# Kernel tuning notes

Measured on AMD Instinct MI355X. Metric: run time of the kernel, lower is better.

The kernel has to match this reference:

```python
import jax, jax.numpy as jnp
import numpy as np

B, H, W, C = 4, 256, 256, 96
NH, WIN = 3, 8
HD = C // NH
HID = 4 * C
SCALE = HD ** -0.5
N = WIN * WIN


def _rel_pos_index(win):
    # matches torch.meshgrid([h, w]) default 'ij' indexing
    coords = np.stack(np.meshgrid(np.arange(win), np.arange(win), indexing='ij'))
    cf = coords.reshape(2, -1)
    rel = (cf[:, :, None] - cf[:, None, :]).transpose(1, 2, 0).astype(np.int64)
    rel[..., 0] += win - 1
    rel[..., 1] += win - 1
    rel[..., 0] *= 2 * win - 1
    return rel.sum(-1)

REL_IDX = jnp.asarray(_rel_pos_index(WIN))


def _ln(x, g, b, eps=1e-5):
    m = x.mean(-1, keepdims=True)
    v = ((x - m) ** 2).mean(-1, keepdims=True)
    return (x - m) * jax.lax.rsqrt(v + eps) * g + b


def setup_inputs() -> dict:
    key = jax.random.key(0)
    ks = jax.random.split(key, 10)
    s = 0.02
    return {
        'x': jax.random.normal(ks[0], (B, H * W, C), jnp.float32),
        'g1': jnp.ones((C,), jnp.float32), 'b1': jnp.zeros((C,), jnp.float32),
        'wq': jax.random.normal(ks[1], (C, C), jnp.float32) * s, 'bq': jnp.zeros((C,), jnp.float32),
        'wkv': jax.random.normal(ks[2], (C, 2 * C), jnp.float32) * s, 'bkv': jnp.zeros((2 * C,), jnp.float32),
        'rpb': jax.random.normal(ks[3], ((2 * WIN - 1) ** 2, NH), jnp.float32) * s,
        'wp': jax.random.normal(ks[4], (C, C), jnp.float32) * s, 'bp': jnp.zeros((C,), jnp.float32),
        'g2': jnp.ones((C,), jnp.float32), 'b2': jnp.zeros((C,), jnp.float32),
        'w1': jax.random.normal(ks[5], (C, HID), jnp.float32) * s, 'bl1': jnp.zeros((HID,), jnp.float32),
        'wdw': jax.random.normal(ks[6], (HID, 1, 3, 3), jnp.float32) * s, 'bdw': jnp.zeros((HID,), jnp.float32),
        'w2': jax.random.normal(ks[7], (HID, C), jnp.float32) * s, 'bl2': jnp.zeros((C,), jnp.float32),
    }


def reference(x, g1, b1, wq, bq, wkv, bkv, rpb, wp, bp, g2, b2, w1, bl1, wdw, bdw, w2, bl2):
    shortcut = x
    xn = _ln(x, g1, b1)
    q = xn @ wq + bq                      # (B, L, C)
    kv = xn @ wkv + bkv                   # (B, L, 2C)

    def windows(t, c):
        t = t.reshape(B, H // WIN, WIN, W // WIN, WIN, c)
        return t.transpose(0, 1, 3, 2, 4, 5).reshape(-1, N, c)

    qw = windows(q, C).reshape(-1, N, NH, HD).transpose(0, 2, 1, 3)     # (nB, NH, N, HD)
    kvw = windows(kv, 2 * C).reshape(-1, N, 2, NH, HD).transpose(2, 0, 3, 1, 4)
    kw, vw = kvw[0], kvw[1]

    attn = jnp.einsum('bhnd,bhmd->bhnm', qw * SCALE, kw)                # (nB, NH, N, N)
    bias = rpb[REL_IDX]                                                  # (N, N, NH)
    attn = attn + bias.transpose(2, 0, 1)[None]
    # shift_size=0 -> shift mask is identically zero; adding it is a no-op
    attn = jax.nn.softmax(attn, axis=-1)
    y = jnp.einsum('bhnm,bhmd->bhnd', attn, vw)
    y = y.transpose(0, 2, 1, 3).reshape(-1, N, C)
    y = y @ wp + bp

    # window_reverse
    y = y.reshape(B, H // WIN, W // WIN, WIN, WIN, C)
    y = y.transpose(0, 1, 3, 2, 4, 5).reshape(B, H * W, C)
    x = shortcut + y

    # LeFF: linear1 + GELU -> depthwise 3x3 conv + GELU -> linear2
    xn2 = _ln(x, g2, b2)
    h = jax.nn.gelu(xn2 @ w1 + bl1, approximate=False)                  # (B, L, HID)
    h = h.reshape(B, H, W, HID).transpose(0, 3, 1, 2)                    # NCHW
    h = jax.lax.conv_general_dilated(
        h, wdw, window_strides=(1, 1), padding=((1, 1), (1, 1)),
        dimension_numbers=('NCHW', 'OIHW', 'NCHW'), feature_group_count=HID)
    h = jax.nn.gelu(h + bdw[None, :, None, None], approximate=False)
    h = h.transpose(0, 2, 3, 1).reshape(B, H * W, HID)
    h = h @ w2 + bl2
    return x + h
```

## Files before the change

kernel.cpp:

```cpp
#include <hip/hip_runtime.h>
#include <math.h>


typedef __attribute__((ext_vector_type(8))) short bf16x8;
typedef __attribute__((ext_vector_type(4))) float f32x4;
typedef __attribute__((ext_vector_type(2))) float f32x2;

#define MFMA(a, b, c) __builtin_amdgcn_mfma_f32_16x16x32_bf16((a), (b), (c), 0, 0, 0)

#define WQ_T 0
#define WKV_T 18
#define WP_T 54
#define W1_T 72
#define W2_T 144
#define NTILES_TOT 216

__device__ __forceinline__ unsigned short f2bf(float f) {
  union { float f; unsigned u; } v; v.f = f;
  unsigned r = v.u + 0x7FFFu + ((v.u >> 16) & 1u);
  return (unsigned short)(r >> 16);
}
__device__ __forceinline__ float asf(unsigned u) {
  union { unsigned u; float f; } v; v.u = u; return v.f;
}
__device__ __forceinline__ unsigned cvtpk_bf16(float lo, float hi) {
  unsigned r;
  asm("v_cvt_pk_bf16_f32 %0, %1, %2" : "=v"(r) : "v"(lo), "v"(hi));
  return r;
}
__device__ __forceinline__ float gelu(float x) {
  float t = x * x;
  float w = x * fmaf(t, -0.07135941f, -1.5957691f);
  float a = __expf(w);
  return x * __builtin_amdgcn_rcpf(1.f + a);
}
__device__ __forceinline__ bf16x8 ldw(const unsigned short* wswz, int tile, int lane) {
  return *(const bf16x8*)(wswz + ((size_t)(tile * 64 + lane)) * 8);
}
__device__ __forceinline__ int xcd_swz(int bid) {
  return (bid & 7) * 512 + (bid >> 3);
}

__global__ void kwconv(const float* __restrict__ wq, const float* __restrict__ wkv,
                       const float* __restrict__ wp, const float* __restrict__ w1,
                       const float* __restrict__ w2, const float* __restrict__ wdw,
                       unsigned short* __restrict__ wswz, float* __restrict__ wdwT) {
  int tid = blockIdx.x * 256 + threadIdx.x;
  if (tid >= NTILES_TOT * 64) {
    int i = tid - NTILES_TOT * 64;
    if (i < 3456) {
      int ch = i % 384, tap = i / 384;
      wdwT[tap * 384 + ch] = wdw[ch * 9 + tap];
    }
    return;
  }
  int e = tid; const float* src; int N, NT;
  if (e < 1152)      { src = wq;  N = 96;  NT = 6; }
  else if (e < 3456) { src = wkv; N = 192; NT = 12; e -= 1152; }
  else if (e < 4608) { src = wp;  N = 96;  NT = 6;  e -= 3456; }
  else if (e < 9216) { src = w1;  N = 384; NT = 24; e -= 4608; }
  else               { src = w2;  N = 96;  NT = 6;  e -= 9216; }
  int lane = e & 63, t = e >> 6;
  int nt = t % NT, kt = t / NT;
  int k0 = kt * 32 + (lane >> 4) * 8;
  int n = nt * 16 + (lane & 15);
  unsigned short* dst = wswz + (size_t)tid * 8;
#pragma unroll
  for (int i = 0; i < 8; ++i) dst[i] = f2bf(src[(size_t)(k0 + i) * N + n]);
}

__global__ __launch_bounds__(256) void kattn(
    const float* __restrict__ x, const float* __restrict__ g1, const float* __restrict__ b1,
    const float* __restrict__ bq, const float* __restrict__ bkv,
    const float* __restrict__ rpb, const float* __restrict__ bp,
    const unsigned short* __restrict__ wswz, float* __restrict__ x2) {
  __shared__ __align__(16) unsigned short sm0[4 * 3 * 64 * 8];
  __shared__ __align__(16) unsigned short sm1[24 * 64 * 8];
  __shared__ __align__(16) unsigned short sm2[3 * 2 * 2 * 64 * 8];

  const int tid = threadIdx.x;
  const int lane = tid & 63, w = tid >> 6;
  const int lrow = lane >> 4, lcol = lane & 15;
  const int wi = xcd_swz(blockIdx.x);
  const int b = wi >> 10, wy = (wi >> 5) & 31, wx = wi & 31;

  long rowoff[4];
#pragma unroll
  for (int r = 0; r < 4; ++r) {
    int m = w * 16 + lrow * 4 + r;
    int gy = wy * 8 + (m >> 3), gx = wx * 8 + (m & 7);
    rowoff[r] = ((long)b * 65536 + gy * 256 + gx) * 96;
  }

  float xv[4][6], xn[4][6], gv[6], bv[6];
#pragma unroll
  for (int nt = 0; nt < 6; ++nt) {
    int c = nt * 16 + lcol;
    gv[nt] = g1[c]; bv[nt] = b1[c];
#pragma unroll
    for (int r = 0; r < 4; ++r) xv[r][nt] = x[rowoff[r] + c];
  }
#pragma unroll
  for (int r = 0; r < 4; ++r) {
    float s = 0.f, sq = 0.f;
#pragma unroll
    for (int nt = 0; nt < 6; ++nt) { float v = xv[r][nt]; s += v; sq += v * v; }
#pragma unroll
    for (int off = 1; off <= 8; off <<= 1) { s += __shfl_xor(s, off, 64); sq += __shfl_xor(sq, off, 64); }
    float mean = s * (1.f / 96.f);
    float var = sq * (1.f / 96.f) - mean * mean;
    float rs = rsqrtf(var + 1e-5f);
#pragma unroll
    for (int nt = 0; nt < 6; ++nt) xn[r][nt] = (xv[r][nt] - mean) * rs * gv[nt] + bv[nt];
  }
#pragma unroll
  for (int r = 0; r < 4; ++r) {
    int mm = lrow * 4 + r;
#pragma unroll
    for (int nt = 0; nt < 6; ++nt) {
      int c = nt * 16 + lcol;
      int kt = c >> 5;
      int lanew = mm + (((c & 31) >> 3) << 4);
      sm0[((w * 3 + kt) * 64 + lanew) * 8 + (c & 7)] = f2bf(xn[r][nt]);
    }
  }
  __syncthreads();

  bf16x8 af[3];
#pragma unroll
  for (int kt = 0; kt < 3; ++kt) af[kt] = *(const bf16x8*)(sm0 + ((w * 3 + kt) * 64 + lane) * 8);
  for (int nt = 0; nt < 18; ++nt) {
    f32x4 acc = {0.f, 0.f, 0.f, 0.f};
#pragma unroll
    for (int kt = 0; kt < 3; ++kt) {
      int tile = (nt < 6) ? (WQ_T + kt * 6 + nt) : (WKV_T + kt * 12 + (nt - 6));
      acc = MFMA(af[kt], ldw(wswz, tile, lane), acc);
    }
    int c = nt * 16 + lcol;
#pragma unroll
    for (int r = 0; r < 4; ++r) {
      int m = w * 16 + lrow * 4 + r;
      float val = acc[r];
      if (c < 96) {
        val = (val + bq[c]) * 0.17677669529663687f;
        int head = c >> 5, d = c & 31;
        sm1[((head * 4 + w) * 64 + (m & 15) + ((d >> 3) << 4)) * 8 + (d & 7)] = f2bf(val);
      } else if (c < 192) {
        int kc = c - 96;
        val += bkv[kc];
        int head = kc >> 5, d = kc & 31;
        sm1[((12 + head * 4 + w) * 64 + (m & 15) + ((d >> 3) << 4)) * 8 + (d & 7)] = f2bf(val);
      } else {
        int vc = c - 192;
        val += bkv[96 + vc];
        int head = vc >> 5, d = vc & 31;
        int ktile = m >> 5, nt2 = d >> 4;
        sm2[(((head * 2 + ktile) * 2 + nt2) * 64 + (d & 15) + (((m & 31) >> 3) << 4)) * 8 + (m & 7)] = f2bf(val);
      }
    }
  }
  __syncthreads();

  f32x4 sc[3][4];
#pragma unroll
  for (int uu = 0; uu < 3; ++uu) {
    int u = w * 3 + uu, head = u >> 2, mtq = u & 3;
    bf16x8 aq = *(const bf16x8*)(sm1 + ((head * 4 + mtq) * 64 + lane) * 8);
#pragma unroll
    for (int nt = 0; nt < 4; ++nt) {
      bf16x8 bk = *(const bf16x8*)(sm1 + ((12 + head * 4 + nt) * 64 + lane) * 8);
      f32x4 z = {0.f, 0.f, 0.f, 0.f};
      sc[uu][nt] = MFMA(aq, bk, z);
    }
  }
  __syncthreads();

#pragma unroll
  for (int uu = 0; uu < 3; ++uu) {
    int u = w * 3 + uu, head = u >> 2, mtq = u & 3;
#pragma unroll
    for (int nt = 0; nt < 4; ++nt) {
      int ktok = nt * 16 + lcol;
#pragma unroll
      for (int r = 0; r < 4; ++r) {
        int qtok = mtq * 16 + lrow * 4 + r;
        int dy = (qtok >> 3) - (ktok >> 3) + 7;
        int dx = (qtok & 7) - (ktok & 7) + 7;
        sc[uu][nt][r] += rpb[(dy * 15 + dx) * 3 + head];
      }
    }
#pragma unroll
    for (int r = 0; r < 4; ++r) {
      float mx = fmaxf(fmaxf(sc[uu][0][r], sc[uu][1][r]), fmaxf(sc[uu][2][r], sc[uu][3][r]));
#pragma unroll
      for (int off = 1; off <= 8; off <<= 1) mx = fmaxf(mx, __shfl_xor(mx, off, 64));
      float p[4], sum = 0.f;
#pragma unroll
      for (int nt = 0; nt < 4; ++nt) { p[nt] = __expf(sc[uu][nt][r] - mx); sum += p[nt]; }
#pragma unroll
      for (int off = 1; off <= 8; off <<= 1) sum += __shfl_xor(sum, off, 64);
      float inv = 1.f / sum;
#pragma unroll
      for (int nt = 0; nt < 4; ++nt) sc[uu][nt][r] = p[nt] * inv;
    }
#pragma unroll
    for (int nt = 0; nt < 4; ++nt) {
      int ktok = nt * 16 + lcol;
      int ktile = ktok >> 5, lhi = (ktok & 31) >> 3;
#pragma unroll
      for (int r = 0; r < 4; ++r) {
        int mm = lrow * 4 + r;
        sm1[(((head * 4 + mtq) * 2 + ktile) * 64 + mm + (lhi << 4)) * 8 + (ktok & 7)] = f2bf(sc[uu][nt][r]);
      }
    }
  }
  __syncthreads();

#pragma unroll
  for (int uu = 0; uu < 3; ++uu) {
    int u = w * 3 + uu, head = u >> 2, mtq = u & 3;
#pragma unroll
    for (int nt2 = 0; nt2 < 2; ++nt2) {
      f32x4 acc = {0.f, 0.f, 0.f, 0.f};
#pragma unroll
      for (int ktile = 0; ktile < 2; ++ktile) {
        bf16x8 ap = *(const bf16x8*)(sm1 + (((head * 4 + mtq) * 2 + ktile) * 64 + lane) * 8);
        bf16x8 bv8 = *(const bf16x8*)(sm2 + (((head * 2 + ktile) * 2 + nt2) * 64 + lane) * 8);
        acc = MFMA(ap, bv8, acc);
      }
      int d0 = nt2 * 16 + lcol;
#pragma unroll
      for (int r = 0; r < 4; ++r) {
        int mm = lrow * 4 + r;
        sm0[((mtq * 3 + head) * 64 + mm + ((d0 >> 3) << 4)) * 8 + (d0 & 7)] = f2bf(acc[r]);
      }
    }
  }
  __syncthreads();

  bf16x8 ay[3];
#pragma unroll
  for (int kt = 0; kt < 3; ++kt) ay[kt] = *(const bf16x8*)(sm0 + ((w * 3 + kt) * 64 + lane) * 8);
#pragma unroll
  for (int nt = 0; nt < 6; ++nt) {
    f32x4 acc = {0.f, 0.f, 0.f, 0.f};
#pragma unroll
    for (int kt = 0; kt < 3; ++kt) acc = MFMA(ay[kt], ldw(wswz, WP_T + kt * 6 + nt, lane), acc);
    int c = nt * 16 + lcol;
    float bpc = bp[c];
#pragma unroll
    for (int r = 0; r < 4; ++r) x2[rowoff[r] + c] = acc[r] + bpc + xv[r][nt];
  }
}

__device__ __forceinline__ bf16x8 dwconv_gelu(const uint4* cur,
    const float* wsh, const float* wb, int ch) {
  f32x2 a2[4];
#pragma unroll
  for (int j = 0; j < 4; ++j) a2[j] = (f32x2){0.f, 0.f};
#pragma unroll
  for (int t = 0; t < 9; ++t) {
    f32x4 wlo = *(const f32x4*)(wsh + t * 384 + ch);
    f32x4 whi = *(const f32x4*)(wsh + t * 384 + ch + 4);
    const unsigned* du = (const unsigned*)(cur + t);
    f32x2 d0 = { asf(du[0] << 16), asf(du[0] & 0xffff0000u) };
    f32x2 d1 = { asf(du[1] << 16), asf(du[1] & 0xffff0000u) };
    f32x2 d2 = { asf(du[2] << 16), asf(du[2] & 0xffff0000u) };
    f32x2 d3 = { asf(du[3] << 16), asf(du[3] & 0xffff0000u) };
    f32x2 w0 = {wlo.x, wlo.y}, w1 = {wlo.z, wlo.w};
    f32x2 w2v = {whi.x, whi.y}, w3 = {whi.z, whi.w};
    a2[0] += d0 * w0; a2[1] += d1 * w1; a2[2] += d2 * w2v; a2[3] += d3 * w3;
  }
  f32x4 blo = *(const f32x4*)(wb + ch);
  f32x4 bhi = *(const f32x4*)(wb + ch + 4);
  union { unsigned u[4]; bf16x8 v; } pk;
  pk.u[0] = cvtpk_bf16(gelu(a2[0].x + blo.x), gelu(a2[0].y + blo.y));
  pk.u[1] = cvtpk_bf16(gelu(a2[1].x + blo.z), gelu(a2[1].y + blo.w));
  pk.u[2] = cvtpk_bf16(gelu(a2[2].x + bhi.x), gelu(a2[2].y + bhi.y));
  pk.u[3] = cvtpk_bf16(gelu(a2[3].x + bhi.z), gelu(a2[3].y + bhi.w));
  return pk.v;
}

__global__ __launch_bounds__(256) void kleff(
    const float* __restrict__ x2, const float* __restrict__ g2,
    const float* __restrict__ b2, const float* __restrict__ bl1,
    const float* __restrict__ wdwT, const float* __restrict__ bdw,
    const float* __restrict__ bl2, const unsigned short* __restrict__ wswz,
    float* __restrict__ out) {
  __shared__ __align__(16) unsigned short xn_lds[21 * 64 * 8];
  __shared__ __align__(16) unsigned short h_lds[100 * 200];
  __shared__ __align__(16) float wsh[9 * 384 + 384];

  const int tid = threadIdx.x, lane = tid & 63, w = tid >> 6;
  const int lrow = lane >> 4, lcol = lane & 15;
  const int bid = xcd_swz(blockIdx.x);
  const int b = bid >> 10, ty0 = ((bid >> 5) & 31) * 8, tx0 = (bid & 31) * 8;

  for (int i = tid; i < 960; i += 256) {
    float4 v = (i < 864) ? ((const float4*)wdwT)[i] : ((const float4*)bdw)[i - 864];
    ((float4*)wsh)[i] = v;
  }
  const float* wb = wsh + 3456;

  const int mt1 = (w < 3) ? 4 + w : 3;
  unsigned vmask = 0;

  {
    float gv[6], bv[6];
#pragma unroll
    for (int nt = 0; nt < 6; ++nt) { gv[nt] = g2[nt * 16 + lcol]; bv[nt] = b2[nt * 16 + lcol]; }
#pragma unroll
    for (int mi = 0; mi < 2; ++mi) {
      const int mt = mi ? mt1 : w;
      float xv[4][6];
#pragma unroll
      for (int r = 0; r < 4; ++r) {
        int t = mt * 16 + lrow * 4 + r;
        int hy = (t * 205) >> 11, hx = t - hy * 10;
        int gy = ty0 - 1 + hy, gx = tx0 - 1 + hx;
        bool ok = ((unsigned)gy < 256u) && ((unsigned)gx < 256u) && (t < 100);
        vmask |= (ok ? 1u : 0u) << (mi * 4 + r);
        int cgy = min(max(gy, 0), 255), cgx = min(max(gx, 0), 255);
        long roff = ((long)b * 65536 + cgy * 256 + cgx) * 96;
#pragma unroll
        for (int nt = 0; nt < 6; ++nt) xv[r][nt] = x2[roff + nt * 16 + lcol];
      }
#pragma unroll
      for (int r = 0; r < 4; ++r) {
        float s = 0.f, sq = 0.f;
#pragma unroll
        for (int nt = 0; nt < 6; ++nt) { float v = xv[r][nt]; s += v; sq += v * v; }
#pragma unroll
        for (int off = 1; off <= 8; off <<= 1) { s += __shfl_xor(s, off, 64); sq += __shfl_xor(sq, off, 64); }
        float mean = s * (1.f / 96.f);
        float var = sq * (1.f / 96.f) - mean * mean;
        float rs = rsqrtf(var + 1e-5f);
        int mm = lrow * 4 + r;
#pragma unroll
        for (int nt = 0; nt < 6; ++nt) {
          float val = (xv[r][nt] - mean) * rs * gv[nt] + bv[nt];
          int c = nt * 16 + lcol;
          int kt = c >> 5;
          int lanew = mm + (((c & 31) >> 3) << 4);
          xn_lds[((mt * 3 + kt) * 64 + lanew) * 8 + (c & 7)] = f2bf(val);
        }
      }
    }
  }
  __syncthreads();

  f32x4 acc[6];
#pragma unroll
  for (int nt = 0; nt < 6; ++nt) { f32x4 z = {0.f, 0.f, 0.f, 0.f}; acc[nt] = z; }

  bf16x8 af0[3], af1[3];
#pragma unroll
  for (int kt = 0; kt < 3; ++kt) {
    af0[kt] = *(const bf16x8*)(xn_lds + ((w * 3 + kt) * 64 + lane) * 8);
    af1[kt] = *(const bf16x8*)(xn_lds + ((mt1 * 3 + kt) * 64 + lane) * 8);
  }

  const int pint = w * 16 + lcol;
  const int iy = pint >> 3, ix = pint & 7;
  const int cg0 = lrow * 8;
  const int hbase = ((iy * 10) + ix) * 200 + cg0;

#pragma unroll
  for (int H = 0; H < 2; ++H) {
#pragma unroll
    for (int ntl = 0; ntl < 12; ++ntl) {
      int nt = H * 12 + ntl;
      bf16x8 wf0 = ldw(wswz, W1_T + 0 * 24 + nt, lane);
      bf16x8 wf1 = ldw(wswz, W1_T + 1 * 24 + nt, lane);
      bf16x8 wf2 = ldw(wswz, W1_T + 2 * 24 + nt, lane);
      float bb = bl1[H * 192 + ntl * 16 + lcol];
      f32x4 a0 = {0.f, 0.f, 0.f, 0.f}, a1 = {0.f, 0.f, 0.f, 0.f};
      a0 = MFMA(af0[0], wf0, a0); a0 = MFMA(af0[1], wf1, a0); a0 = MFMA(af0[2], wf2, a0);
      a1 = MFMA(af1[0], wf0, a1); a1 = MFMA(af1[1], wf1, a1); a1 = MFMA(af1[2], wf2, a1);
#pragma unroll
      for (int r = 0; r < 4; ++r) {
        int t0 = w * 16 + lrow * 4 + r;
        if (t0 < 100) {
          unsigned short hv = ((vmask >> r) & 1u) ? f2bf(gelu(a0[r] + bb)) : (unsigned short)0;
          h_lds[t0 * 200 + ntl * 16 + lcol] = hv;
        }
        int t1 = mt1 * 16 + lrow * 4 + r;
        if (t1 < 100) {
          unsigned short hv = ((vmask >> (4 + r)) & 1u) ? f2bf(gelu(a1[r] + bb)) : (unsigned short)0;
          h_lds[t1 * 200 + ntl * 16 + lcol] = hv;
        }
      }
    }
    __syncthreads();

#pragma unroll
    for (int ktl = 0; ktl < 6; ++ktl) {
      int chl = ktl * 32 + cg0;
      uint4 dv[9];
#pragma unroll
      for (int dy = 0; dy < 3; ++dy)
#pragma unroll
        for (int dx = 0; dx < 3; ++dx)
          dv[dy * 3 + dx] = *(const uint4*)(h_lds + hbase + dy * 2000 + dx * 200 + ktl * 32);
      bf16x8 pk = dwconv_gelu(dv, wsh, wb, H * 192 + chl);
      int ktg = H * 6 + ktl;
#pragma unroll
      for (int nt = 0; nt < 6; ++nt)
        acc[nt] = MFMA(pk, ldw(wswz, W2_T + ktg * 6 + nt, lane), acc[nt]);
    }
    __syncthreads();
  }

#pragma unroll
  for (int nt = 0; nt < 6; ++nt) {
    int c = nt * 16 + lcol;
    float bb = bl2[c];
#pragma unroll
    for (int r = 0; r < 4; ++r) {
      int mm = w * 16 + lrow * 4 + r;
      int oy = ty0 + (mm >> 3), ox = tx0 + (mm & 7);
      long row = (long)b * 65536 + oy * 256 + ox;
      out[row * 96 + c] = acc[nt][r] + bb + x2[row * 96 + c];
    }
  }
}

extern "C" void kernel_launch(void* const* d_in, const int* in_sizes, int n_in,
                              void* d_out, int out_size, void* d_ws, size_t ws_size,
                              hipStream_t stream) {
  const float* x   = (const float*)d_in[0];
  const float* g1  = (const float*)d_in[1];
  const float* b1  = (const float*)d_in[2];
  const float* wq  = (const float*)d_in[3];
  const float* bq  = (const float*)d_in[4];
  const float* wkv = (const float*)d_in[5];
  const float* bkv = (const float*)d_in[6];
  const float* rpb = (const float*)d_in[7];
  const float* wp  = (const float*)d_in[8];
  const float* bp  = (const float*)d_in[9];
  const float* g2  = (const float*)d_in[10];
  const float* b2  = (const float*)d_in[11];
  const float* w1  = (const float*)d_in[12];
  const float* bl1 = (const float*)d_in[13];
  const float* wdw = (const float*)d_in[14];
  const float* bdw = (const float*)d_in[15];
  const float* w2  = (const float*)d_in[16];
  const float* bl2 = (const float*)d_in[17];

  char* ws = (char*)d_ws;
  unsigned short* wswz = (unsigned short*)ws;
  float* wdwT = (float*)(ws + (size_t)(256 << 10));
  float* x2 = (float*)(ws + (size_t)(4 << 20));
  float* outp = (float*)d_out;

  kwconv<<<68, 256, 0, stream>>>(wq, wkv, wp, w1, w2, wdw, wswz, wdwT);
  kattn<<<4096, 256, 0, stream>>>(x, g1, b1, bq, bkv, rpb, bp, wswz, x2);
  kleff<<<4096, 256, 0, stream>>>(x2, g2, b2, bl1, wdwT, bdw, bl2, wswz, outp);
}
```

Before: 565.8 us.

## Shrink LeFF LDS footprint with aliased buffer and channel-group layout for occupancy

```diff
diff --git a/kernel.cpp b/kernel.cpp
--- a/kernel.cpp
+++ b/kernel.cpp
@@ -253,26 +253,35 @@
   }
 }
 
-__device__ __forceinline__ bf16x8 dwconv_gelu(const uint4* cur,
-    const float* wsh, const float* wb, int ch) {
+__device__ __forceinline__ bf16x8 dwconv_gelu_g(
+    const unsigned short* h00,
+    const float* __restrict__ wdwT, const float* __restrict__ bdw, int ch) {
   f32x2 a2[4];
 #pragma unroll
   for (int j = 0; j < 4; ++j) a2[j] = (f32x2){0.f, 0.f};
 #pragma unroll
-  for (int t = 0; t < 9; ++t) {
-    f32x4 wlo = *(const f32x4*)(wsh + t * 384 + ch);
-    f32x4 whi = *(const f32x4*)(wsh + t * 384 + ch + 4);
-    const unsigned* du = (const unsigned*)(cur + t);
-    f32x2 d0 = { asf(du[0] << 16), asf(du[0] & 0xffff0000u) };
-    f32x2 d1 = { asf(du[1] << 16), asf(du[1] & 0xffff0000u) };
-    f32x2 d2 = { asf(du[2] << 16), asf(du[2] & 0xffff0000u) };
-    f32x2 d3 = { asf(du[3] << 16), asf(du[3] & 0xffff0000u) };
-    f32x2 w0 = {wlo.x, wlo.y}, w1 = {wlo.z, wlo.w};
-    f32x2 w2v = {whi.x, whi.y}, w3 = {whi.z, whi.w};
-    a2[0] += d0 * w0; a2[1] += d1 * w1; a2[2] += d2 * w2v; a2[3] += d3 * w3;
-  }
-  f32x4 blo = *(const f32x4*)(wb + ch);
-  f32x4 bhi = *(const f32x4*)(wb + ch + 4);
+  for (int dy = 0; dy < 3; ++dy) {
+    uint4 dv[3];
+#pragma unroll
+    for (int dx = 0; dx < 3; ++dx)
+      dv[dx] = *(const uint4*)(h00 + (dy * 10 + dx) * 8);
+#pragma unroll
+    for (int dx = 0; dx < 3; ++dx) {
+      int t = dy * 3 + dx;
+      f32x4 wlo = *(const f32x4*)(wdwT + t * 384 + ch);
+      f32x4 whi = *(const f32x4*)(wdwT + t * 384 + ch + 4);
+      const unsigned* du = (const unsigned*)&dv[dx];
+      f32x2 d0 = { asf(du[0] << 16), asf(du[0] & 0xffff0000u) };
+      f32x2 d1 = { asf(du[1] << 16), asf(du[1] & 0xffff0000u) };
+      f32x2 d2 = { asf(du[2] << 16), asf(du[2] & 0xffff0000u) };
+      f32x2 d3 = { asf(du[3] << 16), asf(du[3] & 0xffff0000u) };
+      f32x2 w0 = {wlo.x, wlo.y}, w1 = {wlo.z, wlo.w};
+      f32x2 w2v = {whi.x, whi.y}, w3 = {whi.z, whi.w};
+      a2[0] += d0 * w0; a2[1] += d1 * w1; a2[2] += d2 * w2v; a2[3] += d3 * w3;
+    }
+  }
+  f32x4 blo = *(const f32x4*)(bdw + ch);
+  f32x4 bhi = *(const f32x4*)(bdw + ch + 4);
   union { unsigned u[4]; bf16x8 v; } pk;
   pk.u[0] = cvtpk_bf16(gelu(a2[0].x + blo.x), gelu(a2[0].y + blo.y));
   pk.u[1] = cvtpk_bf16(gelu(a2[1].x + blo.z), gelu(a2[1].y + blo.w));
@@ -281,26 +290,18 @@
   return pk.v;
 }
 
-__global__ __launch_bounds__(256) void kleff(
+__global__ __launch_bounds__(256, 3) void kleff(
     const float* __restrict__ x2, const float* __restrict__ g2,
     const float* __restrict__ b2, const float* __restrict__ bl1,
     const float* __restrict__ wdwT, const float* __restrict__ bdw,
     const float* __restrict__ bl2, const unsigned short* __restrict__ wswz,
     float* __restrict__ out) {
-  __shared__ __align__(16) unsigned short xn_lds[21 * 64 * 8];
-  __shared__ __align__(16) unsigned short h_lds[100 * 200];
-  __shared__ __align__(16) float wsh[9 * 384 + 384];
+  __shared__ __align__(16) unsigned short smem[24 * 808];
 
   const int tid = threadIdx.x, lane = tid & 63, w = tid >> 6;
   const int lrow = lane >> 4, lcol = lane & 15;
   const int bid = xcd_swz(blockIdx.x);
   const int b = bid >> 10, ty0 = ((bid >> 5) & 31) * 8, tx0 = (bid & 31) * 8;
-
-  for (int i = tid; i < 960; i += 256) {
-    float4 v = (i < 864) ? ((const float4*)wdwT)[i] : ((const float4*)bdw)[i - 864];
-    ((float4*)wsh)[i] = v;
-  }
-  const float* wb = wsh + 3456;
 
   const int mt1 = (w < 3) ? 4 + w : 3;
   unsigned vmask = 0;
@@ -342,52 +343,54 @@
           int c = nt * 16 + lcol;
           int kt = c >> 5;
           int lanew = mm + (((c & 31) >> 3) << 4);
-          xn_lds[((mt * 3 + kt) * 64 + lanew) * 8 + (c & 7)] = f2bf(val);
+          smem[((mt * 3 + kt) * 64 + lanew) * 8 + (c & 7)] = f2bf(val);
         }
       }
     }
   }
   __syncthreads();
 
+  bf16x8 af0[3], af1[3];
+#pragma unroll
+  for (int kt = 0; kt < 3; ++kt) {
+    af0[kt] = *(const bf16x8*)(smem + ((w * 3 + kt) * 64 + lane) * 8);
+    af1[kt] = *(const bf16x8*)(smem + ((mt1 * 3 + kt) * 64 + lane) * 8);
+  }
+  __syncthreads();
+
   f32x4 acc[6];
 #pragma unroll
   for (int nt = 0; nt < 6; ++nt) { f32x4 z = {0.f, 0.f, 0.f, 0.f}; acc[nt] = z; }
-
-  bf16x8 af0[3], af1[3];
-#pragma unroll
-  for (int kt = 0; kt < 3; ++kt) {
-    af0[kt] = *(const bf16x8*)(xn_lds + ((w * 3 + kt) * 64 + lane) * 8);
-    af1[kt] = *(const bf16x8*)(xn_lds + ((mt1 * 3 + kt) * 64 + lane) * 8);
-  }
 
   const int pint = w * 16 + lcol;
   const int iy = pint >> 3, ix = pint & 7;
   const int cg0 = lrow * 8;
-  const int hbase = ((iy * 10) + ix) * 200 + cg0;
 
 #pragma unroll
   for (int H = 0; H < 2; ++H) {
 #pragma unroll
     for (int ntl = 0; ntl < 12; ++ntl) {
       int nt = H * 12 + ntl;
-      bf16x8 wf0 = ldw(wswz, W1_T + 0 * 24 + nt, lane);
-      bf16x8 wf1 = ldw(wswz, W1_T + 1 * 24 + nt, lane);
-      bf16x8 wf2 = ldw(wswz, W1_T + 2 * 24 + nt, lane);
+      bf16x8 wf0 = ldw(wswz, W1_T + nt, lane);
+      bf16x8 wf1 = ldw(wswz, W1_T + 24 + nt, lane);
+      bf16x8 wf2 = ldw(wswz, W1_T + 48 + nt, lane);
       float bb = bl1[H * 192 + ntl * 16 + lcol];
       f32x4 a0 = {0.f, 0.f, 0.f, 0.f}, a1 = {0.f, 0.f, 0.f, 0.f};
       a0 = MFMA(af0[0], wf0, a0); a0 = MFMA(af0[1], wf1, a0); a0 = MFMA(af0[2], wf2, a0);
       a1 = MFMA(af1[0], wf0, a1); a1 = MFMA(af1[1], wf1, a1); a1 = MFMA(af1[2], wf2, a1);
+      const int g = ntl * 2 + (lcol >> 3);
+      const int e = lcol & 7;
 #pragma unroll
       for (int r = 0; r < 4; ++r) {
         int t0 = w * 16 + lrow * 4 + r;
         if (t0 < 100) {
           unsigned short hv = ((vmask >> r) & 1u) ? f2bf(gelu(a0[r] + bb)) : (unsigned short)0;
-          h_lds[t0 * 200 + ntl * 16 + lcol] = hv;
+          smem[g * 808 + t0 * 8 + e] = hv;
         }
         int t1 = mt1 * 16 + lrow * 4 + r;
         if (t1 < 100) {
           unsigned short hv = ((vmask >> (4 + r)) & 1u) ? f2bf(gelu(a1[r] + bb)) : (unsigned short)0;
-          h_lds[t1 * 200 + ntl * 16 + lcol] = hv;
+          smem[g * 808 + t1 * 8 + e] = hv;
         }
       }
     }
@@ -395,14 +398,9 @@
 
 #pragma unroll
     for (int ktl = 0; ktl < 6; ++ktl) {
-      int chl = ktl * 32 + cg0;
-      uint4 dv[9];
-#pragma unroll
-      for (int dy = 0; dy < 3; ++dy)
-#pragma unroll
-        for (int dx = 0; dx < 3; ++dx)
-          dv[dy * 3 + dx] = *(const uint4*)(h_lds + hbase + dy * 2000 + dx * 200 + ktl * 32);
-      bf16x8 pk = dwconv_gelu(dv, wsh, wb, H * 192 + chl);
+      const int g = ktl * 4 + lrow;
+      const unsigned short* h00 = smem + g * 808 + (iy * 10 + ix) * 8;
+      bf16x8 pk = dwconv_gelu_g(h00, wdwT, bdw, H * 192 + ktl * 32 + cg0);
       int ktg = H * 6 + ktl;
 #pragma unroll
       for (int nt = 0; nt < 6; ++nt)
```

After: 587.9 us. +3.9%, slower.
